# Optimization experiments

Measured on AMD Instinct MI355X. Metric: run time of the kernel, lower is better.

## Reference

```python
import jax, jax.numpy as jnp
import numpy as np

B, D = 65536, 365

def _linp(k, fan_in, fan_out):
    # torch nn.Linear default init: U(-1/sqrt(fan_in), 1/sqrt(fan_in))
    kw, kb = jax.random.split(k)
    bound = 1.0 / np.sqrt(fan_in)
    W = jax.random.uniform(kw, (fan_in, fan_out), jnp.float32, -bound, bound)
    b = jax.random.uniform(kb, (fan_out,), jnp.float32, -bound, bound)
    return W, b

def setup_inputs() -> dict:
    key = jax.random.key(0)
    ks = jax.random.split(key, 9)
    x = jax.random.normal(ks[0], (B, D), jnp.float32)
    W1, b1 = _linp(ks[1], D, 512)
    W2, b2 = _linp(ks[2], 512, 256)
    W3, b3 = _linp(ks[3], 256, 128)
    Ws, bs = _linp(ks[4], 6, 32)
    Wc1, bc1 = _linp(ks[5], 128 + 32, 64)
    Wc2, bc2 = _linp(ks[6], 64, 32)
    Wc3, bc3 = _linp(ks[7], 32, 1)
    return dict(x=x, W1=W1, b1=b1, W2=W2, b2=b2, W3=W3, b3=b3,
                Ws=Ws, bs=bs, Wc1=Wc1, bc1=bc1, Wc2=Wc2, bc2=bc2,
                Wc3=Wc3, bc3=bc3)

def _row_stats(x):
    # fused row-wise moments: mean, std (ddof=1), min, max, skew, kurtosis
    mu = jnp.mean(x, axis=1, keepdims=True)          # [B,1]
    c = x - mu                                        # [B,D]
    var1 = jnp.sum(c * c, axis=1) / (x.shape[1] - 1)  # unbiased, matches torch.std()
    sigma = jnp.sqrt(var1)
    m3 = jnp.mean(c ** 3, axis=1)
    m4 = jnp.mean(c ** 4, axis=1)
    skew = m3 / (sigma ** 3 + 1e-8)
    kurt = m4 / (sigma ** 4 + 1e-8)
    return jnp.stack([mu[:, 0], sigma, jnp.min(x, axis=1), jnp.max(x, axis=1), skew, kurt], axis=1)

def reference(x, W1, b1, W2, b2, W3, b3, Ws, bs, Wc1, bc1, Wc2, bc2, Wc3, bc3):
    h = jax.nn.relu(x @ W1 + b1)
    h = jax.nn.relu(h @ W2 + b2)
    seq = jax.nn.relu(h @ W3 + b3)            # [B,128]
    stat = _row_stats(x) @ Ws + bs            # [B,32]
    comb = jnp.concatenate([seq, stat], axis=1)
    c = jax.nn.relu(comb @ Wc1 + bc1)
    c = jax.nn.relu(c @ Wc2 + bc2)
    out = jax.nn.sigmoid(c @ Wc3 + bc3)       # [B,1]
    return out[:, 0]
```

## Files before the change

### kernel.cpp

```cpp
#include <hip/hip_runtime.h>
#include <math.h>

typedef __attribute__((ext_vector_type(8)))  short short8;
typedef __attribute__((ext_vector_type(16))) float float16;

#define DEVI __device__ __forceinline__

DEVI short f2bf(float f) {
    unsigned u = __float_as_uint(f);
    u = (u + 0x7fffu + ((u >> 16) & 1u)) >> 16;
    return (short)u;
}
DEVI unsigned pk2(float a, float b) {
    return (unsigned)(unsigned short)f2bf(a) | ((unsigned)(unsigned short)f2bf(b) << 16);
}
DEVI float16 mfma16(short8 a, short8 b, float16 c) {
    return __builtin_amdgcn_mfma_f32_32x32x16_bf16(a, b, c, 0, 0, 0);
}
DEVI int rowof(int r, int h) { return (r & 3) + 8 * (r >> 2) + 4 * h; }
DEVI short8 lds8(const short* p) { return *(const short8*)p; }
DEVI short8 gld8(const short* p) { return *(const short8*)p; }

#define W1T_OFF  0
#define W2T_OFF  188416
#define W3T_OFF  319488
#define WC1T_OFF 352256
#define WC2T_OFF 362496

__global__ void prep_v2(const float* __restrict__ W1, const float* __restrict__ W2,
                        const float* __restrict__ W3, const float* __restrict__ Wc1,
                        const float* __restrict__ Wc2, short* __restrict__ ws) {
    __shared__ short T[16 * 72];
    int b = blockIdx.x, t = threadIdx.x;
    const float* src; int K, N; size_t base; int kc, nb;
    if (b < 184)        {            src = W1;  K = 365; N = 512; base = W1T_OFF;  kc = b >> 3;  nb = b & 7; }
    else if (b < 312)   { int l = b - 184; src = W2;  K = 512; N = 256; base = W2T_OFF;  kc = l >> 2;  nb = l & 3; }
    else if (b < 344)   { int l = b - 312; src = W3;  K = 256; N = 128; base = W3T_OFF;  kc = l >> 1;  nb = l & 1; }
    else if (b < 354)   {            src = Wc1; K = 160; N = 64;  base = WC1T_OFF; kc = b - 344; nb = 0; }
    else                {            src = Wc2; K = 64;  N = 32;  base = WC2T_OFF; kc = b - 354; nb = 0; }
    int n = nb * 64 + (t & 63);
    int kr = t >> 6;
    #pragma unroll
    for (int i = 0; i < 4; ++i) {
        int krow = kr + 4 * i;
        int k = kc * 16 + krow;
        float v = (k < K && n < N) ? src[(size_t)k * N + n] : 0.f;
        T[krow * 72 + (t & 63)] = f2bf(v);
    }
    __syncthreads();
    int n2 = t >> 2, ksq = (t & 3) * 4;
    int ng = nb * 64 + n2;
    if (ng < N) {
        unsigned lo = (unsigned)(unsigned short)T[ksq * 72 + n2]
                    | ((unsigned)(unsigned short)T[(ksq + 1) * 72 + n2] << 16);
        unsigned hi = (unsigned)(unsigned short)T[(ksq + 2) * 72 + n2]
                    | ((unsigned)(unsigned short)T[(ksq + 3) * 72 + n2] << 16);
        uint2 d; d.x = lo; d.y = hi;
        *(uint2*)(ws + base + ((size_t)kc * N + ng) * 16 + ksq) = d;
    }
}

__global__ __launch_bounds__(512, 4)
void fused_v4(const float* __restrict__ x,
              const float* __restrict__ b1f, const float* __restrict__ b2f,
              const float* __restrict__ b3f, const float* __restrict__ Wsf,
              const float* __restrict__ bsf, const float* __restrict__ bc1f,
              const float* __restrict__ bc2f, const float* __restrict__ Wc3f,
              const float* __restrict__ bc3f,
              const short* __restrict__ wsw, float* __restrict__ out)
{
    __shared__ __align__(16) char smem[65536];
    short* XT    = (short*)smem;
    short* SB    = (short*)(smem + 48128);
    short* C1    = (short*)smem;
    short* FEATL = (short*)(smem + 12288);
    float* C2    = (float*)(smem + 20480);

    const short* W1t  = wsw + W1T_OFF;
    const short* W2t  = wsw + W2T_OFF;
    const short* W3t  = wsw + W3T_OFF;
    const short* Wc1t = wsw + WC1T_OFF;
    const short* Wc2t = wsw + WC2T_OFF;

    const int tid  = (int)threadIdx.x;
    const int lane = tid & 63;
    const int wv   = tid >> 6;
    const int m    = lane & 31;
    const int h    = lane >> 5;
    const int rowBase = (int)blockIdx.x * 64;

    float bb1a = b1f[32 * wv + m];
    float bb1b = b1f[256 + 32 * wv + m];
    float bb2  = b2f[32 * wv + m];
    float bb3  = b3f[32 * (wv & 3) + m];

    const int r0 = tid >> 3, j0 = tid & 7;
    const float* xrow = x + (size_t)(rowBase + r0) * 365;
    float s1 = 0.f, s2 = 0.f, s3 = 0.f, s4 = 0.f, mn = 1e30f, mx = -1e30f;
    #pragma unroll
    for (int i = 0; i < 6; ++i) {
        int o = j0 + 8 * i;
        if (o <= 45) {
            float xf[8];
            #pragma unroll
            for (int jj = 0; jj < 8; ++jj) {
                int col = o * 8 + jj;
                xf[jj] = (col < 365) ? xrow[col] : 0.f;
            }
            #pragma unroll
            for (int jj = 0; jj < 8; ++jj) {
                int col = o * 8 + jj;
                if (col < 365) {
                    float v = xf[jj], v2 = v * v;
                    s1 += v; s2 += v2; s3 += v2 * v; s4 += v2 * v2;
                    mn = fminf(mn, v); mx = fmaxf(mx, v);
                }
            }
            int4 w4;
            w4.x = (int)pk2(xf[0], xf[1]); w4.y = (int)pk2(xf[2], xf[3]);
            w4.z = (int)pk2(xf[4], xf[5]); w4.w = (int)pk2(xf[6], xf[7]);
            *(int4*)(XT + r0 * 376 + o * 8) = w4;
        }
    }
    #pragma unroll
    for (int off = 1; off <= 4; off <<= 1) {
        s1 += __shfl_xor(s1, off); s2 += __shfl_xor(s2, off);
        s3 += __shfl_xor(s3, off); s4 += __shfl_xor(s4, off);
        mn = fminf(mn, __shfl_xor(mn, off)); mx = fmaxf(mx, __shfl_xor(mx, off));
    }
    unsigned fdw0, fdw1;
    {
        float mean  = s1 * (1.0f / 365.0f);
        float var1  = (s2 - 365.0f * mean * mean) * (1.0f / 364.0f);
        float sigma = sqrtf(var1);
        float m3 = (s3 - 3.0f * mean * s2) * (1.0f / 365.0f) + 2.0f * mean * mean * mean;
        float mm = mean * mean;
        float m4 = (s4 - 4.0f * mean * s3 + 6.0f * mm * s2) * (1.0f / 365.0f) - 3.0f * mm * mm;
        float sg2 = sigma * sigma;
        float skew = m3 / (sigma * sg2 + 1e-8f);
        float kurt = m4 / (sg2 * sg2 + 1e-8f);
        float st[6] = { mean, sigma, mn, mx, skew, kurt };
        float f[4];
        #pragma unroll
        for (int c0 = 0; c0 < 4; ++c0) {
            int c = 4 * j0 + c0;
            float acc = bsf[c];
            #pragma unroll
            for (int jj = 0; jj < 6; ++jj) acc += st[jj] * Wsf[jj * 32 + c];
            f[c0] = acc;
        }
        fdw0 = pk2(f[0], f[1]); fdw1 = pk2(f[2], f[3]);
    }
    __syncthreads();

    float16 ha0, ha1;
    #pragma unroll
    for (int i = 0; i < 16; ++i) { ha0[i] = 0.f; ha1[i] = 0.f; }

    const short* Ap0  = XT + m * 376 + h * 8;
    const short* Ap1  = XT + (32 + m) * 376 + h * 8;
    const short* A2p0 = SB + m * 136 + h * 8;
    const short* A2p1 = SB + (32 + m) * 136 + h * 8;
    const int stcol = 32 * (wv & 3) + m;

    #pragma unroll
    for (int p = 0; p < 2; ++p) {
        float16 ga0, ga1;
        #pragma unroll
        for (int i = 0; i < 16; ++i) { ga0[i] = 0.f; ga1[i] = 0.f; }
        const short* B1 = W1t + (256 * p + 32 * wv + m) * 16 + h * 8;
        #pragma unroll
        for (int kc = 0; kc < 23; ++kc) {
            short8 b  = gld8(B1 + kc * 8192);
            short8 a0 = lds8(Ap0 + kc * 16);
            short8 a1 = lds8(Ap1 + kc * 16);
            ga0 = mfma16(a0, b, ga0);
            ga1 = mfma16(a1, b, ga1);
        }
        float bb = p ? bb1b : bb1a;
        #pragma unroll
        for (int s = 0; s < 2; ++s) {
            int sl = 2 * p + s;
            __syncthreads();
            if ((wv >> 2) == s) {
                #pragma unroll
                for (int r = 0; r < 16; ++r) {
                    SB[rowof(r, h) * 136 + stcol]        = f2bf(fmaxf(ga0[r] + bb, 0.f));
                    SB[(32 + rowof(r, h)) * 136 + stcol] = f2bf(fmaxf(ga1[r] + bb, 0.f));
                }
            }
            __syncthreads();
            const short* B2 = W2t + sl * 8 * 4096 + (32 * wv + m) * 16 + h * 8;
            #pragma unroll
            for (int i = 0; i < 8; ++i) {
                short8 b  = gld8(B2 + i * 4096);
                short8 a0 = lds8(A2p0 + i * 16);
                short8 a1 = lds8(A2p1 + i * 16);
                ha0 = mfma16(a0, b, ha0);
                ha1 = mfma16(a1, b, ha1);
            }
        }
    }

    float16 g3;
    #pragma unroll
    for (int i = 0; i < 16; ++i) g3[i] = 0.f;
    const short* A3p = SB + ((wv >> 2) * 32 + m) * 136 + h * 8;
    #pragma unroll
    for (int t = 0; t < 2; ++t) {
        __syncthreads();
        if ((wv >> 2) == t) {
            #pragma unroll
            for (int r = 0; r < 16; ++r) {
                SB[rowof(r, h) * 136 + stcol]        = f2bf(fmaxf(ha0[r] + bb2, 0.f));
                SB[(32 + rowof(r, h)) * 136 + stcol] = f2bf(fmaxf(ha1[r] + bb2, 0.f));
            }
        }
        __syncthreads();
        const short* B3 = W3t + t * 8 * 2048 + (32 * (wv & 3) + m) * 16 + h * 8;
        #pragma unroll
        for (int i = 0; i < 8; ++i) {
            short8 b = gld8(B3 + i * 2048);
            short8 a = lds8(A3p + i * 16);
            g3 = mfma16(a, b, g3);
        }
    }

    __syncthreads();
    {
        int rb = (wv >> 2) * 32;
        #pragma unroll
        for (int r = 0; r < 16; ++r)
            SB[(rb + rowof(r, h)) * 136 + stcol] = f2bf(fmaxf(g3[r] + bb3, 0.f));
        *(unsigned*)(FEATL + r0 * 40 + 4 * j0)     = fdw0;
        *(unsigned*)(FEATL + r0 * 40 + 4 * j0 + 2) = fdw1;
    }
    __syncthreads();

    if (wv < 4) {
        int m4 = wv & 1, c4 = wv >> 1;
        const short* B4 = Wc1t + (32 * c4 + m) * 16 + h * 8;
        const short* A4 = SB + (m4 * 32 + m) * 136 + h * 8;
        float16 g4;
        #pragma unroll
        for (int i = 0; i < 16; ++i) g4[i] = 0.f;
        #pragma unroll
        for (int i = 0; i < 8; ++i) {
            short8 b = gld8(B4 + i * 1024);
            short8 a = lds8(A4 + i * 16);
            g4 = mfma16(a, b, g4);
        }
        const short* AF = FEATL + (m4 * 32 + m) * 40 + h * 8;
        #pragma unroll
        for (int i = 0; i < 2; ++i) {
            short8 b = gld8(B4 + (8 + i) * 1024);
            short8 a = lds8(AF + i * 16);
            g4 = mfma16(a, b, g4);
        }
        float bb = bc1f[32 * c4 + m];
        #pragma unroll
        for (int r = 0; r < 16; ++r)
            C1[(m4 * 32 + rowof(r, h)) * 72 + 32 * c4 + m] = f2bf(fmaxf(g4[r] + bb, 0.f));
    }
    __syncthreads();

    if (wv < 2) {
        const short* B5 = Wc2t + m * 16 + h * 8;
        const short* A5 = C1 + (wv * 32 + m) * 72 + h * 8;
        float16 g5;
        #pragma unroll
        for (int i = 0; i < 16; ++i) g5[i] = 0.f;
        #pragma unroll
        for (int i = 0; i < 4; ++i) {
            short8 b = gld8(B5 + i * 512);
            short8 a = lds8(A5 + i * 16);
            g5 = mfma16(a, b, g5);
        }
        float bb = bc2f[m];
        #pragma unroll
        for (int r = 0; r < 16; ++r)
            C2[(wv * 32 + rowof(r, h)) * 33 + m] = fmaxf(g5[r] + bb, 0.f);
    }
    __syncthreads();

    if (tid < 64) {
        float z = bc3f[0];
        #pragma unroll
        for (int i = 0; i < 32; ++i) z += C2[tid * 33 + i] * Wc3f[i];
        out[rowBase + tid] = 1.0f / (1.0f + expf(-z));
    }
}

extern "C" void kernel_launch(void* const* d_in, const int* in_sizes, int n_in,
                              void* d_out, int out_size, void* d_ws, size_t ws_size,
                              hipStream_t stream)
{
    (void)in_sizes; (void)n_in; (void)out_size; (void)ws_size;
    const float* x   = (const float*)d_in[0];
    const float* W1  = (const float*)d_in[1];
    const float* b1  = (const float*)d_in[2];
    const float* W2  = (const float*)d_in[3];
    const float* b2  = (const float*)d_in[4];
    const float* W3  = (const float*)d_in[5];
    const float* b3  = (const float*)d_in[6];
    const float* Ws  = (const float*)d_in[7];
    const float* bs  = (const float*)d_in[8];
    const float* Wc1 = (const float*)d_in[9];
    const float* bc1 = (const float*)d_in[10];
    const float* Wc2 = (const float*)d_in[11];
    const float* bc2 = (const float*)d_in[12];
    const float* Wc3 = (const float*)d_in[13];
    const float* bc3 = (const float*)d_in[14];
    short* ws = (short*)d_ws;

    prep_v2<<<358, 256, 0, stream>>>(W1, W2, W3, Wc1, Wc2, ws);
    fused_v4<<<1024, 512, 0, stream>>>(x, b1, b2, b3, Ws, bs, bc1, bc2, Wc3, bc3,
                                       ws, (float*)d_out);
}
```

Measured before the change: 238.1 us.

## Precompute bf16 x and row-stat features in prep kernel, read from workspace

Extends the weight-prep kernel with extra blocks that convert x to padded bf16 rows and compute the row statistics plus the stats linear layer once per row in one pass, using raw power sums. A new main kernel loads the x tiles straight from global memory as MFMA operands instead of staging them in LDS, and takes the stats features from the workspace. This moves conversion and stats work out of the MLP kernel and frees LDS, but adds a full bf16 copy of x through memory and uses a less numerically stable moment formula. The old path stays as a fallback when the workspace is too small.

```diff
diff --git a/kernel.cpp b/kernel.cpp
--- a/kernel.cpp
+++ b/kernel.cpp
@@ -26,12 +26,66 @@
 #define W3T_OFF  319488
 #define WC1T_OFF 352256
 #define WC2T_OFF 362496
-
-__global__ void prep_v2(const float* __restrict__ W1, const float* __restrict__ W2,
-                        const float* __restrict__ W3, const float* __restrict__ Wc1,
-                        const float* __restrict__ Wc2, short* __restrict__ ws) {
+#define XBF_OFF   364544ull
+#define FEATB_OFF 24481792ull
+#define WS_NEED_BYTES ((FEATB_OFF + 65536ull * 32ull) * 2ull)
+
+__global__ void prep_all(const float* __restrict__ W1, const float* __restrict__ W2,
+                         const float* __restrict__ W3, const float* __restrict__ Wc1,
+                         const float* __restrict__ Wc2, const float* __restrict__ x,
+                         const float* __restrict__ Wsf, const float* __restrict__ bsf,
+                         short* __restrict__ ws) {
     __shared__ short T[16 * 72];
     int b = blockIdx.x, t = threadIdx.x;
+    if (b >= 358) {
+        int lane = t & 63;
+        int row  = (b - 358) * 4 + (t >> 6);
+        const float* xr = x + (size_t)row * 365;
+        int c0 = lane * 8;
+        float v[8];
+        float s1 = 0.f, s2 = 0.f, s3 = 0.f, s4 = 0.f, mn = 1e30f, mx = -1e30f;
+        #pragma unroll
+        for (int j = 0; j < 8; ++j) {
+            int c = c0 + j;
+            float f = (c < 365) ? xr[c] : 0.f;
+            v[j] = f;
+            if (c < 365) {
+                float f2 = f * f;
+                s1 += f; s2 += f2; s3 += f2 * f; s4 += f2 * f2;
+                mn = fminf(mn, f); mx = fmaxf(mx, f);
+            }
+        }
+        if (lane < 46) {
+            short8 o;
+            #pragma unroll
+            for (int j = 0; j < 8; ++j) o[j] = f2bf(v[j]);
+            *(short8*)(ws + XBF_OFF + (size_t)row * 368 + c0) = o;
+        }
+        #pragma unroll
+        for (int off = 1; off <= 32; off <<= 1) {
+            s1 += __shfl_xor(s1, off); s2 += __shfl_xor(s2, off);
+            s3 += __shfl_xor(s3, off); s4 += __shfl_xor(s4, off);
+            mn = fminf(mn, __shfl_xor(mn, off)); mx = fmaxf(mx, __shfl_xor(mx, off));
+        }
+        float mean  = s1 * (1.0f / 365.0f);
+        float var1  = (s2 - 365.0f * mean * mean) * (1.0f / 364.0f);
+        float sigma = sqrtf(var1);
+        float m3 = (s3 - 3.0f * mean * s2) * (1.0f / 365.0f) + 2.0f * mean * mean * mean;
+        float mm = mean * mean;
+        float m4v = (s4 - 4.0f * mean * s3 + 6.0f * mm * s2) * (1.0f / 365.0f) - 3.0f * mm * mm;
+        float sg2 = sigma * sigma;
+        float st[6] = { mean, sigma, mn, mx,
+                        m3 / (sigma * sg2 + 1e-8f), m4v / (sg2 * sg2 + 1e-8f) };
+        int c = lane & 31;
+        float fv = bsf[c];
+        #pragma unroll
+        for (int jj = 0; jj < 6; ++jj) fv += st[jj] * Wsf[jj * 32 + c];
+        float fA = __shfl(fv, 2 * (lane & 15));
+        float fB = __shfl(fv, 2 * (lane & 15) + 1);
+        if (lane < 16)
+            *(unsigned*)(ws + FEATB_OFF + (size_t)row * 32 + 2 * lane) = pk2(fA, fB);
+        return;
+    }
     const float* src; int K, N; size_t base; int kc, nb;
     if (b < 184)        {            src = W1;  K = 365; N = 512; base = W1T_OFF;  kc = b >> 3;  nb = b & 7; }
     else if (b < 312)   { int l = b - 184; src = W2;  K = 512; N = 256; base = W2T_OFF;  kc = l >> 2;  nb = l & 3; }
@@ -57,6 +111,160 @@
                     | ((unsigned)(unsigned short)T[(ksq + 3) * 72 + n2] << 16);
         uint2 d; d.x = lo; d.y = hi;
         *(uint2*)(ws + base + ((size_t)kc * N + ng) * 16 + ksq) = d;
+    }
+}
+
+__global__ __launch_bounds__(512, 4)
+void fused_v5(const float* __restrict__ b1f, const float* __restrict__ b2f,
+              const float* __restrict__ b3f, const float* __restrict__ bc1f,
+              const float* __restrict__ bc2f, const float* __restrict__ Wc3f,
+              const float* __restrict__ bc3f,
+              const short* __restrict__ wsw, float* __restrict__ out)
+{
+    __shared__ __align__(16) char smem[68864];
+    short* SB  = (short*)smem;
+    short* SEQ = (short*)(smem + 33792);
+    short* C1  = (short*)(smem + 51200);
+    float* C2  = (float*)(smem + 60416);
+
+    const short* W1t   = wsw + W1T_OFF;
+    const short* W2t   = wsw + W2T_OFF;
+    const short* W3t   = wsw + W3T_OFF;
+    const short* Wc1t  = wsw + WC1T_OFF;
+    const short* Wc2t  = wsw + WC2T_OFF;
+    const short* xbf   = wsw + XBF_OFF;
+    const short* featb = wsw + FEATB_OFF;
+
+    const int tid  = (int)threadIdx.x;
+    const int lane = tid & 63;
+    const int wv   = tid >> 6;
+    const int m    = lane & 31;
+    const int h    = lane >> 5;
+    const int rowBase = (int)blockIdx.x * 64;
+
+    float bb1a = b1f[32 * wv + m];
+    float bb1b = b1f[256 + 32 * wv + m];
+    float bb2  = b2f[32 * wv + m];
+    float bb3  = b3f[32 * (wv & 3) + m];
+
+    const short* Ax0 = xbf + (size_t)(rowBase + m) * 368 + h * 8;
+    const short* Ax1 = Ax0 + 32 * 368;
+
+    float16 ha0, ha1;
+    #pragma unroll
+    for (int i = 0; i < 16; ++i) { ha0[i] = 0.f; ha1[i] = 0.f; }
+
+    const short* A2p0 = SB + m * 264 + h * 8;
+    const short* A2p1 = SB + (32 + m) * 264 + h * 8;
+    const int stcol = 32 * wv + m;
+
+    #pragma unroll
+    for (int p = 0; p < 2; ++p) {
+        float16 ga0, ga1;
+        #pragma unroll
+        for (int i = 0; i < 16; ++i) { ga0[i] = 0.f; ga1[i] = 0.f; }
+        const short* B1 = W1t + (256 * p + 32 * wv + m) * 16 + h * 8;
+        #pragma unroll
+        for (int kc = 0; kc < 23; ++kc) {
+            short8 b  = gld8(B1 + kc * 8192);
+            short8 a0 = gld8(Ax0 + kc * 16);
+            short8 a1 = gld8(Ax1 + kc * 16);
+            ga0 = mfma16(a0, b, ga0);
+            ga1 = mfma16(a1, b, ga1);
+        }
+        float bb = p ? bb1b : bb1a;
+        __syncthreads();
+        #pragma unroll
+        for (int r = 0; r < 16; ++r) {
+            int rw = rowof(r, h);
+            SB[rw * 264 + stcol]        = f2bf(fmaxf(ga0[r] + bb, 0.f));
+            SB[(32 + rw) * 264 + stcol] = f2bf(fmaxf(ga1[r] + bb, 0.f));
+        }
+        __syncthreads();
+        const short* B2 = W2t + p * 16 * 4096 + (32 * wv + m) * 16 + h * 8;
+        #pragma unroll
+        for (int i = 0; i < 16; ++i) {
+            short8 b  = gld8(B2 + i * 4096);
+            short8 a0 = lds8(A2p0 + i * 16);
+            short8 a1 = lds8(A2p1 + i * 16);
+            ha0 = mfma16(a0, b, ha0);
+            ha1 = mfma16(a1, b, ha1);
+        }
+    }
+
+    __syncthreads();
+    #pragma unroll
+    for (int r = 0; r < 16; ++r) {
+        int rw = rowof(r, h);
+        SB[rw * 264 + stcol]        = f2bf(fmaxf(ha0[r] + bb2, 0.f));
+        SB[(32 + rw) * 264 + stcol] = f2bf(fmaxf(ha1[r] + bb2, 0.f));
+    }
+    __syncthreads();
+
+    const int cg3 = wv & 3, rh3 = wv >> 2;
+    float16 g3;
+    #pragma unroll
+    for (int i = 0; i < 16; ++i) g3[i] = 0.f;
+    const short* A3 = SB + (32 * rh3 + m) * 264 + h * 8;
+    const short* B3 = W3t + (32 * cg3 + m) * 16 + h * 8;
+    #pragma unroll
+    for (int i = 0; i < 16; ++i) {
+        short8 b = gld8(B3 + i * 2048);
+        short8 a = lds8(A3 + i * 16);
+        g3 = mfma16(a, b, g3);
+    }
+    #pragma unroll
+    for (int r = 0; r < 16; ++r)
+        SEQ[(32 * rh3 + rowof(r, h)) * 136 + 32 * cg3 + m] = f2bf(fmaxf(g3[r] + bb3, 0.f));
+    __syncthreads();
+
+    if (wv < 4) {
+        int m4 = wv & 1, c4 = wv >> 1;
+        const short* B4 = Wc1t + (32 * c4 + m) * 16 + h * 8;
+        const short* A4 = SEQ + (32 * m4 + m) * 136 + h * 8;
+        float16 g4;
+        #pragma unroll
+        for (int i = 0; i < 16; ++i) g4[i] = 0.f;
+        #pragma unroll
+        for (int i = 0; i < 8; ++i) {
+            short8 b = gld8(B4 + i * 1024);
+            short8 a = lds8(A4 + i * 16);
+            g4 = mfma16(a, b, g4);
+        }
+        const short* AF = featb + (size_t)(rowBase + 32 * m4 + m) * 32 + h * 8;
+        g4 = mfma16(gld8(AF),      gld8(B4 + 8 * 1024), g4);
+        g4 = mfma16(gld8(AF + 16), gld8(B4 + 9 * 1024), g4);
+        float bb = bc1f[32 * c4 + m];
+        #pragma unroll
+        for (int r = 0; r < 16; ++r)
+            C1[(32 * m4 + rowof(r, h)) * 72 + 32 * c4 + m] = f2bf(fmaxf(g4[r] + bb, 0.f));
+    }
+    __syncthreads();
+
+    if (wv < 2) {
+        const short* B5 = Wc2t + m * 16 + h * 8;
+        const short* A5 = C1 + (wv * 32 + m) * 72 + h * 8;
+        float16 g5;
+        #pragma unroll
+        for (int i = 0; i < 16; ++i) g5[i] = 0.f;
+        #pragma unroll
+        for (int i = 0; i < 4; ++i) {
+            short8 b = gld8(B5 + i * 512);
+            short8 a = lds8(A5 + i * 16);
+            g5 = mfma16(a, b, g5);
+        }
+        float bb = bc2f[m];
+        #pragma unroll
+        for (int r = 0; r < 16; ++r)
+            C2[(wv * 32 + rowof(r, h)) * 33 + m] = fmaxf(g5[r] + bb, 0.f);
+    }
+    __syncthreads();
+
+    if (tid < 64) {
+        float z = bc3f[0];
+        #pragma unroll
+        for (int i = 0; i < 32; ++i) z += C2[tid * 33 + i] * Wc3f[i];
+        out[rowBase + tid] = 1.0f / (1.0f + expf(-z));
     }
 }
 
@@ -295,7 +503,7 @@
                               void* d_out, int out_size, void* d_ws, size_t ws_size,
                               hipStream_t stream)
 {
-    (void)in_sizes; (void)n_in; (void)out_size; (void)ws_size;
+    (void)in_sizes; (void)n_in; (void)out_size;
     const float* x   = (const float*)d_in[0];
     const float* W1  = (const float*)d_in[1];
     const float* b1  = (const float*)d_in[2];
@@ -313,7 +521,13 @@
     const float* bc3 = (const float*)d_in[14];
     short* ws = (short*)d_ws;
 
-    prep_v2<<<358, 256, 0, stream>>>(W1, W2, W3, Wc1, Wc2, ws);
-    fused_v4<<<1024, 512, 0, stream>>>(x, b1, b2, b3, Ws, bs, bc1, bc2, Wc3, bc3,
-                                       ws, (float*)d_out);
-}
+    if (ws_size >= WS_NEED_BYTES) {
+        prep_all<<<358 + 16384, 256, 0, stream>>>(W1, W2, W3, Wc1, Wc2, x, Ws, bs, ws);
+        fused_v5<<<1024, 512, 0, stream>>>(b1, b2, b3, bc1, bc2, Wc3, bc3,
+                                           ws, (float*)d_out);
+    } else {
+        prep_all<<<358, 256, 0, stream>>>(W1, W2, W3, Wc1, Wc2, x, Ws, bs, ws);
+        fused_v4<<<1024, 512, 0, stream>>>(x, b1, b2, b3, Ws, bs, bc1, bc2, Wc3, bc3,
+                                           ws, (float*)d_out);
+    }
+}
```

After: 279.8 us. 17.5% more time.
